# Performance work log

Measured on AMD Instinct MI355X. Metric: run time of the kernel, lower is better.

The kernel has to match this reference:

```python
import jax, jax.numpy as jnp
import numpy as np

IN_FEATURES = 2048
OUT_FEATURES = 2048
TOP_K = 1024


def setup_inputs() -> dict:
    key = jax.random.key(0)
    kx, kw, kb = jax.random.split(key, 3)
    bound = 1.0 / np.sqrt(IN_FEATURES)
    x = jax.random.normal(kx, (8, 2048, IN_FEATURES), dtype=jnp.float32)
    weight = jax.random.uniform(kw, (OUT_FEATURES, IN_FEATURES), dtype=jnp.float32,
                                minval=-bound, maxval=bound)
    bias = jax.random.uniform(kb, (OUT_FEATURES,), dtype=jnp.float32,
                              minval=-bound, maxval=bound)
    return {"x": x, "weight": weight, "bias": bias}


def _topk_mask(weight: jnp.ndarray, k: int) -> jnp.ndarray:
    # Per output row, keep the k largest-magnitude weights (binary mask).
    _, idx = jax.lax.top_k(jnp.abs(weight), k)            # [out, k]
    rows = jnp.arange(weight.shape[0])[:, None]            # [out, 1]
    mask = jnp.zeros_like(weight).at[rows, idx].set(1.0)   # scatter ones
    return mask


def reference(x, weight, bias):
    # y = x @ (mask * W)^T + b, mask = top-k by |W| per output feature
    mask = _topk_mask(weight, TOP_K)
    masked_weight = weight * mask                          # [out, in]
    return jnp.einsum('bsi,oi->bso', x, masked_weight) + bias
```

## Files before the change

### kernel.cpp

```cpp
#include <hip/hip_runtime.h>

typedef __attribute__((ext_vector_type(8))) short s16x8;
typedef __attribute__((ext_vector_type(4))) float f32x4;
typedef __attribute__((ext_vector_type(8))) unsigned short u16x8;

#define GLB(p) ((const __attribute__((address_space(1))) void*)(p))
#define LDS(p) ((__attribute__((address_space(3))) void*)(p))

#define BAR() __builtin_amdgcn_s_barrier()
#define VMC(n) asm volatile("s_waitcnt vmcnt(" #n ")" ::: "memory")

__device__ __forceinline__ unsigned short f2bf(float f) {
  unsigned u = __float_as_uint(f);
  u += 0x7fffu + ((u >> 16) & 1u);
  return (unsigned short)(u >> 16);
}

__global__ __launch_bounds__(256) void prep_kernel(
    const float* __restrict__ W, unsigned short* __restrict__ Wb,
    const float* __restrict__ X, unsigned short* __restrict__ Xb) {
  __shared__ int hist[4096];
  __shared__ int scanres[2];
  __shared__ int wsum[4];
  const int tid  = threadIdx.x;

  if (blockIdx.x >= 2048) {
    const size_t i = ((size_t)(blockIdx.x - 2048) * 256 + tid) * 8;
    const float4* xp = (const float4*)(X + i);
    const float4 a = xp[0], b = xp[1];
    u16x8 o;
    o[0] = f2bf(a.x); o[1] = f2bf(a.y); o[2] = f2bf(a.z); o[3] = f2bf(a.w);
    o[4] = f2bf(b.x); o[5] = f2bf(b.y); o[6] = f2bf(b.z); o[7] = f2bf(b.w);
    *(u16x8*)(Xb + i) = o;
    return;
  }

  const int lane = tid & 63;
  const int wv   = tid >> 6;
  const int row  = blockIdx.x;
  const float* wr = W + (size_t)row * 2048;

  const float4 v0 = *(const float4*)(wr + tid * 8);
  const float4 v1 = *(const float4*)(wr + tid * 8 + 4);
  float val[8] = {v0.x, v0.y, v0.z, v0.w, v1.x, v1.y, v1.z, v1.w};
  unsigned key[8];
#pragma unroll
  for (int e = 0; e < 8; ++e) key[e] = __float_as_uint(val[e]) & 0x7fffffffu;

  unsigned prefix = 0;
  int rem = 1024;

  for (int i = tid; i < 4096; i += 256) hist[i] = 0;
  __syncthreads();
#pragma unroll
  for (int e = 0; e < 8; ++e) atomicAdd(&hist[key[e] >> 20], 1);
  __syncthreads();
  if (wv == 0) {
    const int base = 4096 - (lane + 1) * 64;
    int s = 0;
    for (int b = 0; b < 64; ++b) s += hist[base + b];
    int cum = s;
#pragma unroll
    for (int off = 1; off < 64; off <<= 1) {
      int o = __shfl_up(cum, off, 64);
      if (lane >= off) cum += o;
    }
    const int cumex = cum - s;
    if (cumex < rem && rem <= cum) {
      int running = cumex;
      for (int b = 63; b >= 0; --b) {
        int h = hist[base + b];
        if (running + h >= rem) { scanres[0] = base + b; scanres[1] = rem - running; break; }
        running += h;
      }
    }
  }
  __syncthreads();
  prefix = ((unsigned)scanres[0]) << 20;
  rem = scanres[1];
  __syncthreads();

  for (int i = tid; i < 1024; i += 256) hist[i] = 0;
  __syncthreads();
#pragma unroll
  for (int e = 0; e < 8; ++e)
    if ((key[e] >> 20) == (prefix >> 20)) atomicAdd(&hist[(key[e] >> 10) & 1023], 1);
  __syncthreads();
  if (wv == 0) {
    const int base = 1024 - (lane + 1) * 16;
    int s = 0;
    for (int b = 0; b < 16; ++b) s += hist[base + b];
    int cum = s;
#pragma unroll
    for (int off = 1; off < 64; off <<= 1) {
      int o = __shfl_up(cum, off, 64);
      if (lane >= off) cum += o;
    }
    const int cumex = cum - s;
    if (cumex < rem && rem <= cum) {
      int running = cumex;
      for (int b = 15; b >= 0; --b) {
        int h = hist[base + b];
        if (running + h >= rem) { scanres[0] = base + b; scanres[1] = rem - running; break; }
        running += h;
      }
    }
  }
  __syncthreads();
  prefix |= ((unsigned)scanres[0]) << 10;
  rem = scanres[1];
  __syncthreads();

  for (int i = tid; i < 1024; i += 256) hist[i] = 0;
  __syncthreads();
#pragma unroll
  for (int e = 0; e < 8; ++e)
    if ((key[e] >> 10) == (prefix >> 10)) atomicAdd(&hist[key[e] & 1023], 1);
  __syncthreads();
  if (wv == 0) {
    const int base = 1024 - (lane + 1) * 16;
    int s = 0;
    for (int b = 0; b < 16; ++b) s += hist[base + b];
    int cum = s;
#pragma unroll
    for (int off = 1; off < 64; off <<= 1) {
      int o = __shfl_up(cum, off, 64);
      if (lane >= off) cum += o;
    }
    const int cumex = cum - s;
    if (cumex < rem && rem <= cum) {
      int running = cumex;
      for (int b = 15; b >= 0; --b) {
        int h = hist[base + b];
        if (running + h >= rem) { scanres[0] = base + b; scanres[1] = rem - running; break; }
        running += h;
      }
    }
  }
  __syncthreads();
  const unsigned T = prefix | (unsigned)scanres[0];
  rem = scanres[1];

  int eqcnt = 0;
#pragma unroll
  for (int e = 0; e < 8; ++e) eqcnt += (key[e] == T) ? 1 : 0;
  int c = eqcnt;
#pragma unroll
  for (int off = 1; off < 64; off <<= 1) {
    int o = __shfl_up(c, off, 64);
    if (lane >= off) c += o;
  }
  if (lane == 63) wsum[wv] = c;
  __syncthreads();
  int wavebase = 0;
  for (int j = 0; j < wv; ++j) wavebase += wsum[j];
  const int myex = wavebase + c - eqcnt;

  u16x8 o;
  int r = 0;
#pragma unroll
  for (int e = 0; e < 8; ++e) {
    const bool iseq = (key[e] == T);
    const bool keep = (key[e] > T) || (iseq && (myex + r) < rem);
    r += iseq ? 1 : 0;
    o[e] = keep ? f2bf(val[e]) : (unsigned short)0;
  }
  *(u16x8*)(Wb + (size_t)row * 2048 + tid * 8) = o;
}

__global__ __launch_bounds__(512, 2) void gemm_bt_kernel(
    const unsigned short* __restrict__ A,
    const unsigned short* __restrict__ B,
    const float* __restrict__ bias,
    float* __restrict__ C) {
  constexpr int K = 2048;
  constexpr int N = 2048;
  constexpr int T = K / 64;
  constexpr size_t HK = (size_t)128 * K;

  __shared__ __align__(16) char lds_[131072];

  const int tid = threadIdx.x;
  const int l   = tid & 63;
  const int wv  = tid >> 6;
  const int wm  = wv & 1;
  const int wn  = wv >> 1;

  const int lin = blockIdx.x;
  const int o   = (lin & 7) * 64 + (lin >> 3);
  const int tm  = o >> 3;
  const int tn  = o & 7;

  int rS[2], cS[2];
#pragma unroll
  for (int e = 0; e < 2; ++e) {
    const int d   = (e * 512 + tid) * 16;
    const int off = d ^ (((d >> 9) & 1) << 5);
    rS[e] = ((off >> 11) << 4) | ((off >> 6) & 15);
    cS[e] = (((off >> 10) & 1) << 5) | (((off >> 4) & 3) << 3);
  }
  const unsigned short* const pA0 = A + (size_t)(tm * 256 + rS[0]) * K + cS[0];
  const unsigned short* const pA1 = A + (size_t)(tm * 256 + rS[1]) * K + cS[1];
  const unsigned short* const pB0 = B + (size_t)(tn * 256 + rS[0]) * K + cS[0];
  const unsigned short* const pB1 = B + (size_t)(tn * 256 + rS[1]) * K + cS[1];

  auto stage = [&](const unsigned short* g0, const unsigned short* g1, char* d) {
    __builtin_amdgcn_global_load_lds(GLB(g0), LDS(d + wv * 1024), 16, 0, 0);
    __builtin_amdgcn_global_load_lds(GLB(g1), LDS(d + 8192 + wv * 1024), 16, 0, 0);
  };

  const int laneoff = (((l & 15) << 6) | ((l >> 4) << 4)) ^ ((l & 8) << 2);
  const char* const aRd = (const char*)lds_ + wm * 2048 + laneoff;
  const char* const bRd = (const char*)lds_ + 65536 + wn * 2048 + laneoff;

  f32x4 acc[8][4] = {};

  stage(pA0,      pA1,      lds_);
  stage(pA0 + HK, pA1 + HK, lds_ + 16384);
  stage(pB0,      pB1,      lds_ + 65536);
  stage(pB0 + HK, pB1 + HK, lds_ + 65536 + 16384);
  VMC(0);
  BAR();

  for (int t = 0; t < T; ++t) {
    const int bb = t & 1;
    const char* aT = aRd + bb * 32768;
    const char* bT = bRd + bb * 32768;
    char* nA = lds_ + (bb ^ 1) * 32768;
    char* nB = lds_ + 65536 + (bb ^ 1) * 32768;

    if (t + 1 < T) {
      const size_t ko = (size_t)(t + 1) * 64;
      stage(pA0 + ko,      pA1 + ko,      nA);
      stage(pA0 + HK + ko, pA1 + HK + ko, nA + 16384);
      stage(pB0 + ko,      pB1 + ko,      nB);
      stage(pB0 + HK + ko, pB1 + HK + ko, nB + 16384);
    }

    s16x8 af[4][2], bLo[2][2], bHi[2][2];

#pragma unroll
    for (int i = 0; i < 4; ++i)
      af[i][0] = *(const s16x8*)(aT + i * 4096);
#pragma unroll
    for (int j = 0; j < 2; ++j)
      bLo[j][0] = *(const s16x8*)(bT + j * 8192);
#pragma unroll
    for (int i = 0; i < 4; ++i)
      af[i][1] = *(const s16x8*)(aT + i * 4096 + 1024);
#pragma unroll
    for (int j = 0; j < 2; ++j)
      bLo[j][1] = *(const s16x8*)(bT + j * 8192 + 1024);
#pragma unroll
    for (int j = 0; j < 2; ++j) {
      bHi[j][0] = *(const s16x8*)(bT + 16384 + j * 8192);
      bHi[j][1] = *(const s16x8*)(bT + 16384 + j * 8192 + 1024);
    }

    __builtin_amdgcn_s_setprio(1);
#pragma unroll
    for (int kk = 0; kk < 2; ++kk)
#pragma unroll
      for (int i = 0; i < 4; ++i)
#pragma unroll
        for (int j = 0; j < 2; ++j)
          acc[i][j] = __builtin_amdgcn_mfma_f32_16x16x32_bf16(af[i][kk], bLo[j][kk], acc[i][j], 0, 0, 0);
    __builtin_amdgcn_s_setprio(0);

    __builtin_amdgcn_s_setprio(1);
#pragma unroll
    for (int kk = 0; kk < 2; ++kk)
#pragma unroll
      for (int i = 0; i < 4; ++i)
#pragma unroll
        for (int j = 0; j < 2; ++j)
          acc[i][j + 2] = __builtin_amdgcn_mfma_f32_16x16x32_bf16(af[i][kk], bHi[j][kk], acc[i][j + 2], 0, 0, 0);
    __builtin_amdgcn_s_setprio(0);

#pragma unroll
    for (int i = 0; i < 4; ++i) {
      af[i][0] = *(const s16x8*)(aT + 16384 + i * 4096);
      af[i][1] = *(const s16x8*)(aT + 16384 + i * 4096 + 1024);
    }

    __builtin_amdgcn_s_setprio(1);
#pragma unroll
    for (int kk = 0; kk < 2; ++kk)
#pragma unroll
      for (int i = 0; i < 4; ++i)
#pragma unroll
        for (int j = 0; j < 2; ++j)
          acc[i + 4][j + 2] = __builtin_amdgcn_mfma_f32_16x16x32_bf16(af[i][kk], bHi[j][kk], acc[i + 4][j + 2], 0, 0, 0);
    __builtin_amdgcn_s_setprio(0);

    __builtin_amdgcn_s_setprio(1);
#pragma unroll
    for (int kk = 0; kk < 2; ++kk)
#pragma unroll
      for (int i = 0; i < 4; ++i)
#pragma unroll
        for (int j = 0; j < 2; ++j)
          acc[i + 4][j] = __builtin_amdgcn_mfma_f32_16x16x32_bf16(af[i][kk], bLo[j][kk], acc[i + 4][j], 0, 0, 0);
    __builtin_amdgcn_s_setprio(0);

    VMC(0);
    BAR();
  }

  float bv[4];
#pragma unroll
  for (int j = 0; j < 4; ++j)
    bv[j] = bias[tn * 256 + (4 * j + wn) * 16 + (l & 15)];

  const int crow0 = tm * 256 + wm * 16 + (l >> 4) * 4;
  const int ccol0 = tn * 256 + wn * 16 + (l & 15);
  float* Cp = C + (size_t)crow0 * N + ccol0;
#pragma unroll
  for (int i = 0; i < 8; ++i)
#pragma unroll
    for (int j = 0; j < 4; ++j)
#pragma unroll
      for (int r = 0; r < 4; ++r)
        Cp[(size_t)(i * 32 + r) * N + j * 64] = acc[i][j][r] + bv[j];
}

extern "C" void kernel_launch(void* const* d_in, const int* in_sizes, int n_in,
                              void* d_out, int out_size, void* d_ws, size_t ws_size,
                              hipStream_t stream) {
  const float* x    = (const float*)d_in[0];
  const float* w    = (const float*)d_in[1];
  const float* bias = (const float*)d_in[2];
  float* out = (float*)d_out;

  constexpr int M = 8 * 2048;
  constexpr int N = 2048;
  constexpr int K = 2048;

  unsigned short* xb = (unsigned short*)d_ws;
  unsigned short* wb = xb + (size_t)M * K;

  const int conv_blocks = ((size_t)M * K) / (256 * 8);
  prep_kernel<<<2048 + conv_blocks, 256, 0, stream>>>(w, wb, x, xb);
  gemm_bt_kernel<<<(M / 256) * (N / 256), 512, 0, stream>>>(xb, wb, bias, out);
}
```

Measured before the change: 352.6 us.

## Load B operand directly from global into double-buffered registers, bypassing LDS

The weight (B) tiles are no longer staged through shared memory. Each lane now loads its MFMA B fragments straight from global memory into a pair of register buffers that alternate across a 2x-unrolled K loop, and only the A tile is staged into LDS. This halves the LDS footprint and removes the B LDS reads, so two workgroups may fit per CU. In exchange it adds register pressure (64 extra VGPRs for the two buffers), issues less coalesced per-lane global loads, and makes the two wm waves fetch the same B data redundantly through the cache.

```diff
diff --git a/kernel.cpp b/kernel.cpp
--- a/kernel.cpp
+++ b/kernel.cpp
@@ -178,7 +178,7 @@
   constexpr int T = K / 64;
   constexpr size_t HK = (size_t)128 * K;
 
-  __shared__ __align__(16) char lds_[131072];
+  __shared__ __align__(16) char lds_[65536];
 
   const int tid = threadIdx.x;
   const int l   = tid & 63;
@@ -201,61 +201,57 @@
   }
   const unsigned short* const pA0 = A + (size_t)(tm * 256 + rS[0]) * K + cS[0];
   const unsigned short* const pA1 = A + (size_t)(tm * 256 + rS[1]) * K + cS[1];
-  const unsigned short* const pB0 = B + (size_t)(tn * 256 + rS[0]) * K + cS[0];
-  const unsigned short* const pB1 = B + (size_t)(tn * 256 + rS[1]) * K + cS[1];
-
-  auto stage = [&](const unsigned short* g0, const unsigned short* g1, char* d) {
+
+  auto stageA = [&](const unsigned short* g0, const unsigned short* g1, char* d) {
     __builtin_amdgcn_global_load_lds(GLB(g0), LDS(d + wv * 1024), 16, 0, 0);
     __builtin_amdgcn_global_load_lds(GLB(g1), LDS(d + 8192 + wv * 1024), 16, 0, 0);
   };
 
+  const unsigned short* pB[4];
+#pragma unroll
+  for (int j = 0; j < 4; ++j)
+    pB[j] = B + (size_t)(tn * 256 + (4 * j + wn) * 16 + (l & 15)) * K + (l >> 4) * 8;
+
   const int laneoff = (((l & 15) << 6) | ((l >> 4) << 4)) ^ ((l & 8) << 2);
   const char* const aRd = (const char*)lds_ + wm * 2048 + laneoff;
-  const char* const bRd = (const char*)lds_ + 65536 + wn * 2048 + laneoff;
 
   f32x4 acc[8][4] = {};
-
-  stage(pA0,      pA1,      lds_);
-  stage(pA0 + HK, pA1 + HK, lds_ + 16384);
-  stage(pB0,      pB1,      lds_ + 65536);
-  stage(pB0 + HK, pB1 + HK, lds_ + 65536 + 16384);
+  s16x8 b0[4][2], b1[4][2];
+
+  stageA(pA0,      pA1,      lds_);
+  stageA(pA0 + HK, pA1 + HK, lds_ + 16384);
+#pragma unroll
+  for (int j = 0; j < 4; ++j) {
+    b0[j][0] = *(const s16x8*)(pB[j]);
+    b0[j][1] = *(const s16x8*)(pB[j] + 32);
+  }
   VMC(0);
   BAR();
 
-  for (int t = 0; t < T; ++t) {
+  auto body = [&](int t, s16x8 (&bcur)[4][2], s16x8 (&bnxt)[4][2]) {
     const int bb = t & 1;
     const char* aT = aRd + bb * 32768;
-    const char* bT = bRd + bb * 32768;
     char* nA = lds_ + (bb ^ 1) * 32768;
-    char* nB = lds_ + 65536 + (bb ^ 1) * 32768;
 
     if (t + 1 < T) {
       const size_t ko = (size_t)(t + 1) * 64;
-      stage(pA0 + ko,      pA1 + ko,      nA);
-      stage(pA0 + HK + ko, pA1 + HK + ko, nA + 16384);
-      stage(pB0 + ko,      pB1 + ko,      nB);
-      stage(pB0 + HK + ko, pB1 + HK + ko, nB + 16384);
-    }
-
-    s16x8 af[4][2], bLo[2][2], bHi[2][2];
+      stageA(pA0 + ko,      pA1 + ko,      nA);
+      stageA(pA0 + HK + ko, pA1 + HK + ko, nA + 16384);
+#pragma unroll
+      for (int j = 0; j < 4; ++j) {
+        bnxt[j][0] = *(const s16x8*)(pB[j] + (t + 1) * 64);
+        bnxt[j][1] = *(const s16x8*)(pB[j] + (t + 1) * 64 + 32);
+      }
+    }
+
+    s16x8 af[4][2];
 
 #pragma unroll
     for (int i = 0; i < 4; ++i)
       af[i][0] = *(const s16x8*)(aT + i * 4096);
 #pragma unroll
-    for (int j = 0; j < 2; ++j)
-      bLo[j][0] = *(const s16x8*)(bT + j * 8192);
-#pragma unroll
     for (int i = 0; i < 4; ++i)
       af[i][1] = *(const s16x8*)(aT + i * 4096 + 1024);
-#pragma unroll
-    for (int j = 0; j < 2; ++j)
-      bLo[j][1] = *(const s16x8*)(bT + j * 8192 + 1024);
-#pragma unroll
-    for (int j = 0; j < 2; ++j) {
-      bHi[j][0] = *(const s16x8*)(bT + 16384 + j * 8192);
-      bHi[j][1] = *(const s16x8*)(bT + 16384 + j * 8192 + 1024);
-    }
 
     __builtin_amdgcn_s_setprio(1);
 #pragma unroll
@@ -264,7 +260,7 @@
       for (int i = 0; i < 4; ++i)
 #pragma unroll
         for (int j = 0; j < 2; ++j)
-          acc[i][j] = __builtin_amdgcn_mfma_f32_16x16x32_bf16(af[i][kk], bLo[j][kk], acc[i][j], 0, 0, 0);
+          acc[i][j] = __builtin_amdgcn_mfma_f32_16x16x32_bf16(af[i][kk], bcur[j][kk], acc[i][j], 0, 0, 0);
     __builtin_amdgcn_s_setprio(0);
 
     __builtin_amdgcn_s_setprio(1);
@@ -274,7 +270,7 @@
       for (int i = 0; i < 4; ++i)
 #pragma unroll
         for (int j = 0; j < 2; ++j)
-          acc[i][j + 2] = __builtin_amdgcn_mfma_f32_16x16x32_bf16(af[i][kk], bHi[j][kk], acc[i][j + 2], 0, 0, 0);
+          acc[i][j + 2] = __builtin_amdgcn_mfma_f32_16x16x32_bf16(af[i][kk], bcur[j + 2][kk], acc[i][j + 2], 0, 0, 0);
     __builtin_amdgcn_s_setprio(0);
 
 #pragma unroll
@@ -290,7 +286,7 @@
       for (int i = 0; i < 4; ++i)
 #pragma unroll
         for (int j = 0; j < 2; ++j)
-          acc[i + 4][j + 2] = __builtin_amdgcn_mfma_f32_16x16x32_bf16(af[i][kk], bHi[j][kk], acc[i + 4][j + 2], 0, 0, 0);
+          acc[i + 4][j + 2] = __builtin_amdgcn_mfma_f32_16x16x32_bf16(af[i][kk], bcur[j + 2][kk], acc[i + 4][j + 2], 0, 0, 0);
     __builtin_amdgcn_s_setprio(0);
 
     __builtin_amdgcn_s_setprio(1);
@@ -300,11 +296,16 @@
       for (int i = 0; i < 4; ++i)
 #pragma unroll
         for (int j = 0; j < 2; ++j)
-          acc[i + 4][j] = __builtin_amdgcn_mfma_f32_16x16x32_bf16(af[i][kk], bLo[j][kk], acc[i + 4][j], 0, 0, 0);
+          acc[i + 4][j] = __builtin_amdgcn_mfma_f32_16x16x32_bf16(af[i][kk], bcur[j][kk], acc[i + 4][j], 0, 0, 0);
     __builtin_amdgcn_s_setprio(0);
 
     VMC(0);
     BAR();
+  };
+
+  for (int t = 0; t < T; t += 2) {
+    body(t,     b0, b1);
+    body(t + 1, b1, b0);
   }
 
   float bv[4];
```

Measured after the change: 441.4 us. +25.2%, slower.

## Switch GEMM inner loop from 16x16x32 to 32x32x16 bf16 MFMA tiles

Applied to the files above, without the earlier changes.

Replaces the per-wave 8x4 grid of 16x16 MFMA accumulators with a 4x2 grid of 32x32x16 MFMA accumulators, changing the LDS read addressing (even/odd halves with XOR swizzle) and the epilogue store mapping. Larger MFMA tiles mean fewer LDS fragment loads per FLOP and fewer issued instructions. The risk is different register pressure and possible LDS bank conflicts with the new read pattern, plus a more scattered output store layout.

```diff
diff --git a/kernel.cpp b/kernel.cpp
--- a/kernel.cpp
+++ b/kernel.cpp
@@ -2,6 +2,7 @@
 
 typedef __attribute__((ext_vector_type(8))) short s16x8;
 typedef __attribute__((ext_vector_type(4))) float f32x4;
+typedef __attribute__((ext_vector_type(16))) float f32x16;
 typedef __attribute__((ext_vector_type(8))) unsigned short u16x8;
 
 #define GLB(p) ((const __attribute__((address_space(1))) void*)(p))
@@ -209,11 +210,14 @@
     __builtin_amdgcn_global_load_lds(GLB(g1), LDS(d + 8192 + wv * 1024), 16, 0, 0);
   };
 
-  const int laneoff = (((l & 15) << 6) | ((l >> 4) << 4)) ^ ((l & 8) << 2);
-  const char* const aRd = (const char*)lds_ + wm * 2048 + laneoff;
-  const char* const bRd = (const char*)lds_ + 65536 + wn * 2048 + laneoff;
-
-  f32x4 acc[8][4] = {};
+  const int loff = ((l & 16) ? 2048 : 0) + ((l & 15) << 6) + ((l & 32) ? 16 : 0);
+  const int xr   = (l & 8) << 2;
+  const char* const aE = (const char*)lds_ + wm * 4096 + ((loff)      ^ xr);
+  const char* const aO = (const char*)lds_ + wm * 4096 + ((loff + 32) ^ xr);
+  const char* const bE = (const char*)lds_ + 65536 + wn * 4096 + ((loff)      ^ xr);
+  const char* const bO = (const char*)lds_ + 65536 + wn * 4096 + ((loff + 32) ^ xr);
+
+  f32x16 acc[4][2] = {};
 
   stage(pA0,      pA1,      lds_);
   stage(pA0 + HK, pA1 + HK, lds_ + 16384);
@@ -224,8 +228,10 @@
 
   for (int t = 0; t < T; ++t) {
     const int bb = t & 1;
-    const char* aT = aRd + bb * 32768;
-    const char* bT = bRd + bb * 32768;
+    const char* aTe = aE + bb * 32768;
+    const char* aTo = aO + bb * 32768;
+    const char* bTe = bE + bb * 32768;
+    const char* bTo = bO + bb * 32768;
     char* nA = lds_ + (bb ^ 1) * 32768;
     char* nB = lds_ + 65536 + (bb ^ 1) * 32768;
 
@@ -237,91 +243,72 @@
       stage(pB0 + HK + ko, pB1 + HK + ko, nB + 16384);
     }
 
-    s16x8 af[4][2], bLo[2][2], bHi[2][2];
-
-#pragma unroll
-    for (int i = 0; i < 4; ++i)
-      af[i][0] = *(const s16x8*)(aT + i * 4096);
-#pragma unroll
-    for (int j = 0; j < 2; ++j)
-      bLo[j][0] = *(const s16x8*)(bT + j * 8192);
-#pragma unroll
-    for (int i = 0; i < 4; ++i)
-      af[i][1] = *(const s16x8*)(aT + i * 4096 + 1024);
-#pragma unroll
-    for (int j = 0; j < 2; ++j)
-      bLo[j][1] = *(const s16x8*)(bT + j * 8192 + 1024);
+    s16x8 af[2][4], bf[2][4];
+
 #pragma unroll
     for (int j = 0; j < 2; ++j) {
-      bHi[j][0] = *(const s16x8*)(bT + 16384 + j * 8192);
-      bHi[j][1] = *(const s16x8*)(bT + 16384 + j * 8192 + 1024);
+      bf[j][0] = *(const s16x8*)(bTe + j * 16384);
+      bf[j][1] = *(const s16x8*)(bTo + j * 16384);
+      bf[j][2] = *(const s16x8*)(bTe + j * 16384 + 1024);
+      bf[j][3] = *(const s16x8*)(bTo + j * 16384 + 1024);
+    }
+#pragma unroll
+    for (int p = 0; p < 2; ++p) {
+      af[p][0] = *(const s16x8*)(aTe + p * 8192);
+      af[p][1] = *(const s16x8*)(aTo + p * 8192);
+      af[p][2] = *(const s16x8*)(aTe + p * 8192 + 1024);
+      af[p][3] = *(const s16x8*)(aTo + p * 8192 + 1024);
     }
 
     __builtin_amdgcn_s_setprio(1);
 #pragma unroll
-    for (int kk = 0; kk < 2; ++kk)
-#pragma unroll
-      for (int i = 0; i < 4; ++i)
+    for (int s = 0; s < 4; ++s)
+#pragma unroll
+      for (int p = 0; p < 2; ++p)
 #pragma unroll
         for (int j = 0; j < 2; ++j)
-          acc[i][j] = __builtin_amdgcn_mfma_f32_16x16x32_bf16(af[i][kk], bLo[j][kk], acc[i][j], 0, 0, 0);
+          acc[p][j] = __builtin_amdgcn_mfma_f32_32x32x16_bf16(af[p][s], bf[j][s], acc[p][j], 0, 0, 0);
     __builtin_amdgcn_s_setprio(0);
 
+#pragma unroll
+    for (int p = 0; p < 2; ++p) {
+      af[p][0] = *(const s16x8*)(aTe + (2 + p) * 8192);
+      af[p][1] = *(const s16x8*)(aTo + (2 + p) * 8192);
+      af[p][2] = *(const s16x8*)(aTe + (2 + p) * 8192 + 1024);
+      af[p][3] = *(const s16x8*)(aTo + (2 + p) * 8192 + 1024);
+    }
+
     __builtin_amdgcn_s_setprio(1);
 #pragma unroll
-    for (int kk = 0; kk < 2; ++kk)
-#pragma unroll
-      for (int i = 0; i < 4; ++i)
+    for (int s = 0; s < 4; ++s)
+#pragma unroll
+      for (int p = 0; p < 2; ++p)
 #pragma unroll
         for (int j = 0; j < 2; ++j)
-          acc[i][j + 2] = __builtin_amdgcn_mfma_f32_16x16x32_bf16(af[i][kk], bHi[j][kk], acc[i][j + 2], 0, 0, 0);
-    __builtin_amdgcn_s_setprio(0);
-
-#pragma unroll
-    for (int i = 0; i < 4; ++i) {
-      af[i][0] = *(const s16x8*)(aT + 16384 + i * 4096);
-      af[i][1] = *(const s16x8*)(aT + 16384 + i * 4096 + 1024);
-    }
-
-    __builtin_amdgcn_s_setprio(1);
-#pragma unroll
-    for (int kk = 0; kk < 2; ++kk)
-#pragma unroll
-      for (int i = 0; i < 4; ++i)
-#pragma unroll
-        for (int j = 0; j < 2; ++j)
-          acc[i + 4][j + 2] = __builtin_amdgcn_mfma_f32_16x16x32_bf16(af[i][kk], bHi[j][kk], acc[i + 4][j + 2], 0, 0, 0);
-    __builtin_amdgcn_s_setprio(0);
-
-    __builtin_amdgcn_s_setprio(1);
-#pragma unroll
-    for (int kk = 0; kk < 2; ++kk)
-#pragma unroll
-      for (int i = 0; i < 4; ++i)
-#pragma unroll
-        for (int j = 0; j < 2; ++j)
-          acc[i + 4][j] = __builtin_amdgcn_mfma_f32_16x16x32_bf16(af[i][kk], bLo[j][kk], acc[i + 4][j], 0, 0, 0);
+          acc[2 + p][j] = __builtin_amdgcn_mfma_f32_32x32x16_bf16(af[p][s], bf[j][s], acc[2 + p][j], 0, 0, 0);
     __builtin_amdgcn_s_setprio(0);
 
     VMC(0);
     BAR();
   }
 
-  float bv[4];
-#pragma unroll
-  for (int j = 0; j < 4; ++j)
-    bv[j] = bias[tn * 256 + (4 * j + wn) * 16 + (l & 15)];
-
-  const int crow0 = tm * 256 + wm * 16 + (l >> 4) * 4;
-  const int ccol0 = tn * 256 + wn * 16 + (l & 15);
+  float bv[2];
+#pragma unroll
+  for (int j = 0; j < 2; ++j)
+    bv[j] = bias[tn * 256 + (j * 4 + wn) * 32 + (l & 31)];
+
+  const int crow0 = tm * 256 + wm * 32 + 4 * (l >> 5);
+  const int ccol0 = tn * 256 + wn * 32 + (l & 31);
   float* Cp = C + (size_t)crow0 * N + ccol0;
 #pragma unroll
-  for (int i = 0; i < 8; ++i)
-#pragma unroll
-    for (int j = 0; j < 4; ++j)
-#pragma unroll
-      for (int r = 0; r < 4; ++r)
-        Cp[(size_t)(i * 32 + r) * N + j * 64] = acc[i][j][r] + bv[j];
+  for (int i = 0; i < 4; ++i)
+#pragma unroll
+    for (int j = 0; j < 2; ++j)
+#pragma unroll
+      for (int g = 0; g < 4; ++g)
+#pragma unroll
+        for (int r4 = 0; r4 < 4; ++r4)
+          Cp[(size_t)(i * 64 + g * 8 + r4) * N + j * 128] = acc[i][j][g * 4 + r4] + bv[j];
 }
 
 extern "C" void kernel_launch(void* const* d_in, const int* in_sizes, int n_in,
```

Result: slower. 365.5 us (+3.7%).
